# Kernel tuning notes

Hardware: AMD Instinct MI355X
Metric: run time of the kernel (lower is better)

Reference implementation:

```python
import jax, jax.numpy as jnp
import numpy as np

B, T, OBS, ACT, LAT = 64, 256, 512, 32, 64
BS, NB = 8, 8  # block side length, number of blocks (sum of sides == LAT)
PHI_OUT = NB * BS * BS


def setup_inputs() -> dict:
    key = jax.random.key(0)
    ks = jax.random.split(key, 6)
    w = lambda k, shape: jax.random.normal(k, shape, jnp.float32) * 0.05
    return {
        "observations": jax.random.normal(ks[0], (B, T, OBS), jnp.float32),
        "actions": jax.random.normal(ks[1], (B, T - 1, ACT), jnp.float32),
        "W_enc": w(ks[2], (OBS, LAT)),
        "b_enc": jnp.zeros((LAT,), jnp.float32),
        "W_dec": w(ks[3], (LAT, OBS)),
        "b_dec": jnp.zeros((OBS,), jnp.float32),
        "W_phi": w(ks[4], (ACT, PHI_OUT)),
        "b_phi": jnp.zeros((PHI_OUT,), jnp.float32),
    }


def _forward(observations, actions, W_enc, b_enc, W_dec, b_dec, W_phi, b_phi):
    Bb, Tt = observations.shape[:2]
    Ta = actions.shape[1]  # Tt - 1

    # h(o_t): encoder applied to flattened (B*T) observations
    latent_obs = (observations.reshape(Bb * Tt, OBS) @ W_enc + b_enc).reshape(Bb, Tt, LAT)

    # rho(g_t) = matrix_exp(block_diag(phi(g_t))). Since the matrix is exactly
    # block-diagonal (sum of block sides == LAT), expm factorizes per block.
    after_phi = actions.reshape(Bb * Ta, ACT) @ W_phi + b_phi  # (N, NB*BS*BS)
    # each block is reshaped (BS,BS) then transposed, as in the torch code
    blocks = after_phi.reshape(Bb * Ta * NB, BS, BS).transpose(0, 2, 1)
    exp_blocks = jax.vmap(jax.scipy.linalg.expm)(blocks)  # (N*NB, BS, BS)
    exp_blocks = exp_blocks.reshape(Bb * Ta, NB, BS, BS)
    rho = jnp.zeros((Bb * Ta, LAT, LAT), after_phi.dtype)
    for k in range(NB):  # small fixed structural loop over blocks
        rho = rho.at[:, k * BS:(k + 1) * BS, k * BS:(k + 1) * BS].set(exp_blocks[:, k])
    rho = rho.reshape(Bb, Ta, LAT, LAT)

    # sequential recurrence: h_{t} = h_{t-1} @ rho_{t-1} (row-vector times matrix)
    h0 = latent_obs[:, 0]  # (B, LAT)

    def step(h, rho_t):
        h_new = jnp.einsum('bl,blm->bm', h, rho_t)
        return h_new, h_new

    _, hs = jax.lax.scan(step, h0, jnp.swapaxes(rho, 0, 1))  # (Ta, B, LAT)
    predicted_latents = jnp.concatenate([h0[:, None], jnp.swapaxes(hs, 0, 1)], axis=1)  # (B, T, LAT)

    predicted_obs = (predicted_latents.reshape(Bb * Tt, LAT) @ W_dec + b_dec).reshape(Bb, Tt, OBS)
    return latent_obs, rho, predicted_latents, predicted_obs


def reference(observations, actions, W_enc, b_enc, W_dec, b_dec, W_phi, b_phi):
    return _forward(observations, actions, W_enc, b_enc, W_dec, b_dec, W_phi, b_phi)
```

## Files before the change

### kernel.cpp

```cpp
#include <hip/hip_runtime.h>

#define B_    64
#define T_    256
#define TA_   255
#define OBS_  512
#define ACT_  32
#define LAT_  64
#define NB_   8
#define BS_   8
#define PHI_  512
#define BT_   16384
#define BTA_  16320
#define CH_   16
#define NCH_  16

#define RHO_OFF   1048576ULL
#define PL_OFF    67895296ULL
#define POBS_OFF  68943872ULL

__global__ __launch_bounds__(256) void enc_kernel(
    const float* __restrict__ obs, const float* __restrict__ W,
    const float* __restrict__ bias, float* __restrict__ latent)
{
    __shared__ float At[64][68];
    __shared__ float Wt[64][64];
    const int tid = threadIdx.x;
    const int c0 = (tid & 15) * 4;
    const int r0 = (tid >> 4) * 4;
    const int row0 = blockIdx.x * 64;

    float4 pa[4], pw[4];
#pragma unroll
    for (int j = 0; j < 4; ++j) {
        int ft = tid + j * 256;
        int k4 = ft & 15, r = ft >> 4;
        pa[j] = *(const float4*)(obs + (size_t)(row0 + r) * OBS_ + k4 * 4);
        int c4 = ft & 15, kk = ft >> 4;
        pw[j] = *(const float4*)(W + (size_t)kk * LAT_ + c4 * 4);
    }

    float acc[4][4];
    float4 bv = *(const float4*)(bias + c0);
#pragma unroll
    for (int i = 0; i < 4; ++i) {
        acc[i][0] = bv.x; acc[i][1] = bv.y; acc[i][2] = bv.z; acc[i][3] = bv.w;
    }

    for (int kc = 0; kc < OBS_; kc += 64) {
#pragma unroll
        for (int j = 0; j < 4; ++j) {
            int ft = tid + j * 256;
            int k4 = ft & 15, r = ft >> 4;
            At[k4 * 4 + 0][r] = pa[j].x;
            At[k4 * 4 + 1][r] = pa[j].y;
            At[k4 * 4 + 2][r] = pa[j].z;
            At[k4 * 4 + 3][r] = pa[j].w;
            int c4 = ft & 15, kk = ft >> 4;
            *(float4*)(&Wt[kk][c4 * 4]) = pw[j];
        }
        __syncthreads();
        if (kc + 64 < OBS_) {
#pragma unroll
            for (int j = 0; j < 4; ++j) {
                int ft = tid + j * 256;
                int k4 = ft & 15, r = ft >> 4;
                pa[j] = *(const float4*)(obs + (size_t)(row0 + r) * OBS_ + kc + 64 + k4 * 4);
                int c4 = ft & 15, kk = ft >> 4;
                pw[j] = *(const float4*)(W + (size_t)(kc + 64 + kk) * LAT_ + c4 * 4);
            }
        }
#pragma unroll 4
        for (int kk = 0; kk < 64; ++kk) {
            float4 a = *(const float4*)(&At[kk][r0]);
            float4 w = *(const float4*)(&Wt[kk][c0]);
            acc[0][0] = fmaf(a.x, w.x, acc[0][0]); acc[0][1] = fmaf(a.x, w.y, acc[0][1]);
            acc[0][2] = fmaf(a.x, w.z, acc[0][2]); acc[0][3] = fmaf(a.x, w.w, acc[0][3]);
            acc[1][0] = fmaf(a.y, w.x, acc[1][0]); acc[1][1] = fmaf(a.y, w.y, acc[1][1]);
            acc[1][2] = fmaf(a.y, w.z, acc[1][2]); acc[1][3] = fmaf(a.y, w.w, acc[1][3]);
            acc[2][0] = fmaf(a.z, w.x, acc[2][0]); acc[2][1] = fmaf(a.z, w.y, acc[2][1]);
            acc[2][2] = fmaf(a.z, w.z, acc[2][2]); acc[2][3] = fmaf(a.z, w.w, acc[2][3]);
            acc[3][0] = fmaf(a.w, w.x, acc[3][0]); acc[3][1] = fmaf(a.w, w.y, acc[3][1]);
            acc[3][2] = fmaf(a.w, w.z, acc[3][2]); acc[3][3] = fmaf(a.w, w.w, acc[3][3]);
        }
        __syncthreads();
    }
#pragma unroll
    for (int i = 0; i < 4; ++i)
        *(float4*)(latent + (size_t)(row0 + r0 + i) * LAT_ + c0) =
            make_float4(acc[i][0], acc[i][1], acc[i][2], acc[i][3]);
}

__device__ __forceinline__ void mm8(float* __restrict__ D,
                                    const float* __restrict__ X,
                                    const float* __restrict__ Y)
{
#pragma unroll
    for (int r = 0; r < 8; ++r)
#pragma unroll
        for (int c = 0; c < 8; ++c) {
            float s = 0.f;
#pragma unroll
            for (int q = 0; q < 8; ++q) s = fmaf(X[r * 8 + q], Y[q * 8 + c], s);
            D[r * 8 + c] = s;
        }
}

__global__ __launch_bounds__(256, 1) void phi_expm_kernel(
    const float* __restrict__ act, const float* __restrict__ Wp,
    const float* __restrict__ bp, float* __restrict__ out_blocks,
    float* __restrict__ rho, int use_ws)
{
    const int bt = blockIdx.x * 256 + threadIdx.x;
    const int k  = blockIdx.y;
    if (bt >= BTA_) return;

    float A[64];
    {
        const float* bpp = bp + k * 64;
#pragma unroll
        for (int p = 0; p < 64; ++p) A[p] = bpp[p];
    }
    const float4* arow4 = (const float4*)(act + (size_t)bt * ACT_);
    const float* wk = Wp + k * 64;
#pragma unroll
    for (int a4 = 0; a4 < ACT_ / 4; ++a4) {
        float4 av = arow4[a4];
        const float* wr = wk + (size_t)(a4 * 4) * PHI_;
#pragma unroll
        for (int p = 0; p < 64; ++p) A[p] = fmaf(av.x, wr[p], A[p]);
        wr += PHI_;
#pragma unroll
        for (int p = 0; p < 64; ++p) A[p] = fmaf(av.y, wr[p], A[p]);
        wr += PHI_;
#pragma unroll
        for (int p = 0; p < 64; ++p) A[p] = fmaf(av.z, wr[p], A[p]);
        wr += PHI_;
#pragma unroll
        for (int p = 0; p < 64; ++p) A[p] = fmaf(av.w, wr[p], A[p]);
    }

#pragma unroll
    for (int r = 0; r < 8; ++r) {
        A[r * 9] *= 0.125f;
#pragma unroll
        for (int c = r + 1; c < 8; ++c) {
            float t = A[r * 8 + c];
            A[r * 8 + c] = 0.125f * A[c * 8 + r];
            A[c * 8 + r] = 0.125f * t;
        }
    }

    float P[64];
#pragma unroll
    for (int i = 0; i < 64; ++i) P[i] = (1.f / 5040.f) * A[i];
#pragma unroll
    for (int d = 0; d < 8; ++d) P[d * 9] += 1.f / 720.f;

    constexpr float COEF[6] = {1.f/120.f, 1.f/24.f, 1.f/6.f, 0.5f, 1.f, 1.f};
#pragma unroll
    for (int it = 0; it < 6; ++it) {
        const float coef = COEF[it];
#pragma unroll
        for (int r = 0; r < 8; ++r) {
            float t[8];
#pragma unroll
            for (int c = 0; c < 8; ++c) {
                float s = 0.f;
#pragma unroll
                for (int q = 0; q < 8; ++q) s = fmaf(P[r * 8 + q], A[q * 8 + c], s);
                t[c] = s;
            }
#pragma unroll
            for (int c = 0; c < 8; ++c) P[r * 8 + c] = t[c];
            P[r * 9] += coef;
        }
    }

    float T[64];
    mm8(T, P, P);
    mm8(P, T, T);
    mm8(T, P, P);

    if (use_ws) {
        float* dst = out_blocks + ((size_t)bt * NB_ + k) * 64;
#pragma unroll
        for (int i = 0; i < 16; ++i)
            ((float4*)dst)[i] = make_float4(T[4*i], T[4*i+1], T[4*i+2], T[4*i+3]);
    } else {
        float* base = rho + ((size_t)bt * LAT_ + k * BS_) * LAT_ + k * BS_;
#pragma unroll
        for (int r = 0; r < 8; ++r) {
            *(float4*)(base + (size_t)r * LAT_)     = make_float4(T[r*8+0], T[r*8+1], T[r*8+2], T[r*8+3]);
            *(float4*)(base + (size_t)r * LAT_ + 4) = make_float4(T[r*8+4], T[r*8+5], T[r*8+6], T[r*8+7]);
        }
    }
}

__global__ __launch_bounds__(256) void rho_write_kernel(
    const float* __restrict__ blocks, float* __restrict__ rho)
{
    size_t idx = (size_t)blockIdx.x * 256 + threadIdx.x;
    int c4 = (int)(idx & 15);
    size_t rowg = idx >> 4;
    int row = (int)(rowg & 63);
    size_t bt = rowg >> 6;
    int k = row >> 3, r = row & 7;
    float4 v = make_float4(0.f, 0.f, 0.f, 0.f);
    if ((c4 >> 1) == k)
        v = ((const float4*)(blocks + ((bt * 8 + (size_t)k) * 64 + (size_t)r * 8)))[c4 & 1];
    ((float4*)rho)[idx] = v;
}

__global__ __launch_bounds__(256) void zero_kernel(float4* __restrict__ p)
{
    p[(size_t)blockIdx.x * 256 + threadIdx.x] = make_float4(0.f, 0.f, 0.f, 0.f);
}

__global__ __launch_bounds__(256) void scan_local_kernel(
    const float* __restrict__ eb, float* __restrict__ pfx)
{
    const int tid = blockIdx.x * 256 + threadIdx.x;
    const int k = tid & 7;
    const int j = (tid >> 3) & 15;
    const int b = tid >> 7;
    const int t0 = j * CH_;
    const int cnt = (TA_ - t0 < CH_) ? (TA_ - t0) : CH_;
    const float* src = eb  + ((size_t)(b * TA_ + t0) * 8 + k) * 64;
    float*       dst = pfx + ((size_t)(b * TA_ + t0) * 8 + k) * 64;

    float R[64];
#pragma unroll
    for (int q = 0; q < 16; ++q) ((float4*)R)[q] = ((const float4*)src)[q];
#pragma unroll
    for (int q = 0; q < 16; ++q) ((float4*)dst)[q] = ((const float4*)R)[q];

    for (int i = 1; i < cnt; ++i) {
        const float* mp = src + (size_t)i * 512;
        float M[64];
#pragma unroll
        for (int q = 0; q < 16; ++q) ((float4*)M)[q] = ((const float4*)mp)[q];
#pragma unroll
        for (int r = 0; r < 8; ++r) {
            float tmp[8];
#pragma unroll
            for (int c = 0; c < 8; ++c) {
                float s = 0.f;
#pragma unroll
                for (int q = 0; q < 8; ++q) s = fmaf(R[r * 8 + q], M[q * 8 + c], s);
                tmp[c] = s;
            }
#pragma unroll
            for (int c = 0; c < 8; ++c) R[r * 8 + c] = tmp[c];
        }
        float* dp = dst + (size_t)i * 512;
#pragma unroll
        for (int q = 0; q < 16; ++q) ((float4*)dp)[q] = ((const float4*)R)[q];
    }
}

__global__ __launch_bounds__(64) void scan_chunk_kernel(
    const float* __restrict__ latent, const float* __restrict__ pfx,
    float* __restrict__ gws, float* __restrict__ pl)
{
    const int tid = blockIdx.x * 64 + threadIdx.x;
    const int k = tid & 7, b = tid >> 3;
    float g[8];
    const float* l0 = latent + (size_t)b * T_ * LAT_ + k * 8;
#pragma unroll
    for (int m = 0; m < 8; ++m) g[m] = l0[m];

    float* pl0 = pl + (size_t)b * T_ * LAT_ + k * 8;
    *(float4*)(pl0)     = make_float4(g[0], g[1], g[2], g[3]);
    *(float4*)(pl0 + 4) = make_float4(g[4], g[5], g[6], g[7]);

    float* gp = gws + ((size_t)(b * NCH_) * 8 + k) * 8;
    *(float4*)(gp)     = make_float4(g[0], g[1], g[2], g[3]);
    *(float4*)(gp + 4) = make_float4(g[4], g[5], g[6], g[7]);

    for (int j = 1; j < NCH_; ++j) {
        const float* cp = pfx + ((size_t)(b * TA_ + j * CH_ - 1) * 8 + k) * 64;
        float C[64];
#pragma unroll
        for (int q = 0; q < 16; ++q) ((float4*)C)[q] = ((const float4*)cp)[q];
        float ng[8];
#pragma unroll
        for (int m = 0; m < 8; ++m) {
            float s = 0.f;
#pragma unroll
            for (int l = 0; l < 8; ++l) s = fmaf(g[l], C[l * 8 + m], s);
            ng[m] = s;
        }
#pragma unroll
        for (int m = 0; m < 8; ++m) g[m] = ng[m];
        float* gq = gws + ((size_t)(b * NCH_ + j) * 8 + k) * 8;
        *(float4*)(gq)     = make_float4(g[0], g[1], g[2], g[3]);
        *(float4*)(gq + 4) = make_float4(g[4], g[5], g[6], g[7]);
    }
}

__global__ __launch_bounds__(256) void scan_emit_kernel(
    const float* __restrict__ pfx, const float* __restrict__ gws,
    float* __restrict__ pl)
{
    const int tid = blockIdx.x * 256 + threadIdx.x;
    const int k = tid & 7;
    const int bt = tid >> 3;
    const int b = bt / TA_;
    const int t = bt - b * TA_;
    const int j = t >> 4;

    float g[8];
    const float* gp = gws + ((size_t)(b * NCH_ + j) * 8 + k) * 8;
    *(float4*)(g)     = *(const float4*)(gp);
    *(float4*)(g + 4) = *(const float4*)(gp + 4);

    const float* lp = pfx + ((size_t)bt * 8 + k) * 64;
    float L[64];
#pragma unroll
    for (int q = 0; q < 16; ++q) ((float4*)L)[q] = ((const float4*)lp)[q];

    float h[8];
#pragma unroll
    for (int m = 0; m < 8; ++m) {
        float s = 0.f;
#pragma unroll
        for (int l = 0; l < 8; ++l) s = fmaf(g[l], L[l * 8 + m], s);
        h[m] = s;
    }
    float* op = pl + ((size_t)b * T_ + t + 1) * LAT_ + k * 8;
    *(float4*)(op)     = make_float4(h[0], h[1], h[2], h[3]);
    *(float4*)(op + 4) = make_float4(h[4], h[5], h[6], h[7]);
}

__device__ __forceinline__ void load_block8(float* __restrict__ dst,
                                            const float* __restrict__ p, int rs)
{
#pragma unroll
    for (int r = 0; r < 8; ++r) {
        float4 x = *(const float4*)(p + (size_t)r * rs);
        float4 y = *(const float4*)(p + (size_t)r * rs + 4);
        dst[r*8+0] = x.x; dst[r*8+1] = x.y; dst[r*8+2] = x.z; dst[r*8+3] = x.w;
        dst[r*8+4] = y.x; dst[r*8+5] = y.y; dst[r*8+6] = y.z; dst[r*8+7] = y.w;
    }
}

__global__ __launch_bounds__(64) void recur_kernel(
    const float* __restrict__ latent, const float* __restrict__ eb,
    int chainA, int chainB, int ts, int rs, float* __restrict__ pl)
{
    const int tid = blockIdx.x * 64 + threadIdx.x;
    const int b = tid >> 3, k = tid & 7;
    const float* e = eb + (size_t)b * (size_t)chainA + (size_t)k * (size_t)chainB;

    float h[8];
    const float* l0 = latent + (size_t)b * T_ * LAT_ + k * 8;
#pragma unroll
    for (int j = 0; j < 8; ++j) h[j] = l0[j];
    float* plp = pl + (size_t)b * T_ * LAT_ + k * 8;
    *(float4*)(plp)     = make_float4(h[0], h[1], h[2], h[3]);
    *(float4*)(plp + 4) = make_float4(h[4], h[5], h[6], h[7]);

    float eA[64], eB[64];
    load_block8(eA, e, rs);

#define STEP_(EBUF)                                                          \
    {                                                                        \
        float nh[8];                                                         \
        _Pragma("unroll")                                                    \
        for (int c = 0; c < 8; ++c) {                                        \
            float s = 0.f;                                                   \
            _Pragma("unroll")                                                \
            for (int r = 0; r < 8; ++r) s = fmaf(h[r], EBUF[r * 8 + c], s);  \
            nh[c] = s;                                                       \
        }                                                                    \
        plp += LAT_;                                                         \
        *(float4*)(plp)     = make_float4(nh[0], nh[1], nh[2], nh[3]);       \
        *(float4*)(plp + 4) = make_float4(nh[4], nh[5], nh[6], nh[7]);       \
        _Pragma("unroll")                                                    \
        for (int j = 0; j < 8; ++j) h[j] = nh[j];                            \
    }

    for (int t = 0; t < TA_; t += 2) {
        int tn = (t + 1 < TA_) ? t + 1 : TA_ - 1;
        load_block8(eB, e + (size_t)tn * ts, rs);
        STEP_(eA);
        if (t + 1 >= TA_) break;
        int tn2 = (t + 2 < TA_) ? t + 2 : TA_ - 1;
        load_block8(eA, e + (size_t)tn2 * ts, rs);
        STEP_(eB);
    }
#undef STEP_
}

__global__ __launch_bounds__(256) void dec_kernel(
    const float* __restrict__ pl, const float* __restrict__ W,
    const float* __restrict__ bias, float* __restrict__ out)
{
    __shared__ float At[64][68];
    __shared__ float Wt[64][64];
    const int tid = threadIdx.x;
    const int c0 = (tid & 15) * 4;
    const int r0 = (tid >> 4) * 4;
    const int row0 = blockIdx.x * 64;
    const int n0 = blockIdx.y * 64;

#pragma unroll
    for (int j = 0; j < 4; ++j) {
        int ft = tid + j * 256;
        int k4 = ft & 15, r = ft >> 4;
        float4 v = *(const float4*)(pl + (size_t)(row0 + r) * LAT_ + k4 * 4);
        At[k4 * 4 + 0][r] = v.x;
        At[k4 * 4 + 1][r] = v.y;
        At[k4 * 4 + 2][r] = v.z;
        At[k4 * 4 + 3][r] = v.w;
        int c4 = ft & 15, kk = ft >> 4;
        *(float4*)(&Wt[kk][c4 * 4]) =
            *(const float4*)(W + (size_t)kk * OBS_ + n0 + c4 * 4);
    }
    __syncthreads();

    float acc[4][4];
    float4 bv = *(const float4*)(bias + n0 + c0);
#pragma unroll
    for (int i = 0; i < 4; ++i) {
        acc[i][0] = bv.x; acc[i][1] = bv.y; acc[i][2] = bv.z; acc[i][3] = bv.w;
    }
#pragma unroll 4
    for (int kk = 0; kk < 64; ++kk) {
        float4 a = *(const float4*)(&At[kk][r0]);
        float4 w = *(const float4*)(&Wt[kk][c0]);
        acc[0][0] = fmaf(a.x, w.x, acc[0][0]); acc[0][1] = fmaf(a.x, w.y, acc[0][1]);
        acc[0][2] = fmaf(a.x, w.z, acc[0][2]); acc[0][3] = fmaf(a.x, w.w, acc[0][3]);
        acc[1][0] = fmaf(a.y, w.x, acc[1][0]); acc[1][1] = fmaf(a.y, w.y, acc[1][1]);
        acc[1][2] = fmaf(a.y, w.z, acc[1][2]); acc[1][3] = fmaf(a.y, w.w, acc[1][3]);
        acc[2][0] = fmaf(a.z, w.x, acc[2][0]); acc[2][1] = fmaf(a.z, w.y, acc[2][1]);
        acc[2][2] = fmaf(a.z, w.z, acc[2][2]); acc[2][3] = fmaf(a.z, w.w, acc[2][3]);
        acc[3][0] = fmaf(a.w, w.x, acc[3][0]); acc[3][1] = fmaf(a.w, w.y, acc[3][1]);
        acc[3][2] = fmaf(a.w, w.z, acc[3][2]); acc[3][3] = fmaf(a.w, w.w, acc[3][3]);
    }
#pragma unroll
    for (int i = 0; i < 4; ++i)
        *(float4*)(out + (size_t)(row0 + r0 + i) * OBS_ + n0 + c0) =
            make_float4(acc[i][0], acc[i][1], acc[i][2], acc[i][3]);
}

extern "C" void kernel_launch(void* const* d_in, const int* in_sizes, int n_in,
                              void* d_out, int out_size, void* d_ws, size_t ws_size,
                              hipStream_t stream)
{
    const float* obs  = (const float*)d_in[0];
    const float* act  = (const float*)d_in[1];
    const float* Wenc = (const float*)d_in[2];
    const float* benc = (const float*)d_in[3];
    const float* Wdec = (const float*)d_in[4];
    const float* bdec = (const float*)d_in[5];
    const float* Wphi = (const float*)d_in[6];
    const float* bphi = (const float*)d_in[7];

    float* out    = (float*)d_out;
    float* latent = out;
    float* rho    = out + RHO_OFF;
    float* pl     = out + PL_OFF;
    float* pobs   = out + POBS_OFF;

    const size_t eb_elems = (size_t)BTA_ * NB_ * 64;
    const size_t need_ws   = eb_elems * sizeof(float);
    const size_t need_scan = (2 * eb_elems + 512 * NCH_ * 8) * sizeof(float);
    const bool use_ws   = (ws_size >= need_ws);
    const bool use_scan = (ws_size >= need_scan);
    float* eb  = (float*)d_ws;
    float* pfx = eb + eb_elems;
    float* gws = pfx + eb_elems;

    hipLaunchKernelGGL(enc_kernel, dim3(BT_ / 64), dim3(256), 0, stream,
                       obs, Wenc, benc, latent);

    if (!use_ws)
        hipLaunchKernelGGL(zero_kernel, dim3(66846720 / 1024), dim3(256), 0, stream,
                           (float4*)rho);
    hipLaunchKernelGGL(phi_expm_kernel, dim3((BTA_ + 255) / 256, NB_), dim3(256), 0, stream,
                       act, Wphi, bphi, eb, rho, (int)use_ws);

    if (use_scan) {
        hipLaunchKernelGGL(scan_local_kernel, dim3(8192 / 256), dim3(256), 0, stream,
                           eb, pfx);
        hipLaunchKernelGGL(scan_chunk_kernel, dim3(8), dim3(64), 0, stream,
                           latent, pfx, gws, pl);
        hipLaunchKernelGGL(scan_emit_kernel, dim3(BTA_ * NB_ / 256), dim3(256), 0, stream,
                           pfx, gws, pl);
    } else if (use_ws) {
        hipLaunchKernelGGL(recur_kernel, dim3(8), dim3(64), 0, stream,
                           latent, eb, TA_ * 512, 64, 512, 8, pl);
    } else {
        hipLaunchKernelGGL(recur_kernel, dim3(8), dim3(64), 0, stream,
                           latent, rho, TA_ * 4096, BS_ * LAT_ + BS_, 4096, LAT_, pl);
    }

    if (use_ws)
        hipLaunchKernelGGL(rho_write_kernel, dim3(66846720 / 1024), dim3(256), 0, stream,
                           eb, rho);

    hipLaunchKernelGGL(dec_kernel, dim3(BT_ / 64, OBS_ / 64), dim3(256), 0, stream,
                       pl, Wdec, bdec, pobs);
}
```

Baseline: 523.9 us.

## Halve scan chunk size, fully unroll local scan, prefetch chunk carries

Shrinks the chunked scan from 16 chunks of 16 steps to 32 chunks of 8 steps, so the local-prefix kernel runs twice as many threads, each with a shorter serial dependency chain, in smaller 128-thread blocks. The fixed-length inner loop is fully unrolled via a macro, with a special case for the short last chunk. The sequential carry kernel now prefetches the next chunk matrix while multiplying the current one, hiding load latency. In exchange the serial carry pass has twice as many steps, and the launch-bounds changes may alter register allocation.

```diff
diff --git a/kernel.cpp b/kernel.cpp
--- a/kernel.cpp
+++ b/kernel.cpp
@@ -11,8 +11,8 @@
 #define PHI_  512
 #define BT_   16384
 #define BTA_  16320
-#define CH_   16
-#define NCH_  16
+#define CH_   8
+#define NCH_  32
 
 #define RHO_OFF   1048576ULL
 #define PL_OFF    67895296ULL
@@ -216,13 +216,38 @@
     p[(size_t)blockIdx.x * 256 + threadIdx.x] = make_float4(0.f, 0.f, 0.f, 0.f);
 }
 
-__global__ __launch_bounds__(256) void scan_local_kernel(
+#define SL_BODY_(I)                                                           \
+    {                                                                         \
+        const float* mp = src + (size_t)(I) * 512;                            \
+        float M[64];                                                          \
+        _Pragma("unroll")                                                     \
+        for (int q = 0; q < 16; ++q) ((float4*)M)[q] = ((const float4*)mp)[q];\
+        _Pragma("unroll")                                                     \
+        for (int r = 0; r < 8; ++r) {                                         \
+            float tmp[8];                                                     \
+            _Pragma("unroll")                                                 \
+            for (int c = 0; c < 8; ++c) {                                     \
+                float s = 0.f;                                                \
+                _Pragma("unroll")                                             \
+                for (int q = 0; q < 8; ++q)                                   \
+                    s = fmaf(R[r * 8 + q], M[q * 8 + c], s);                  \
+                tmp[c] = s;                                                   \
+            }                                                                 \
+            _Pragma("unroll")                                                 \
+            for (int c = 0; c < 8; ++c) R[r * 8 + c] = tmp[c];                \
+        }                                                                     \
+        float* dp = dst + (size_t)(I) * 512;                                  \
+        _Pragma("unroll")                                                     \
+        for (int q = 0; q < 16; ++q) ((float4*)dp)[q] = ((const float4*)R)[q];\
+    }
+
+__global__ __launch_bounds__(128, 1) void scan_local_kernel(
     const float* __restrict__ eb, float* __restrict__ pfx)
 {
-    const int tid = blockIdx.x * 256 + threadIdx.x;
+    const int tid = blockIdx.x * 128 + threadIdx.x;
     const int k = tid & 7;
-    const int j = (tid >> 3) & 15;
-    const int b = tid >> 7;
+    const int j = (tid >> 3) & 31;
+    const int b = tid >> 8;
     const int t0 = j * CH_;
     const int cnt = (TA_ - t0 < CH_) ? (TA_ - t0) : CH_;
     const float* src = eb  + ((size_t)(b * TA_ + t0) * 8 + k) * 64;
@@ -234,31 +259,17 @@
 #pragma unroll
     for (int q = 0; q < 16; ++q) ((float4*)dst)[q] = ((const float4*)R)[q];
 
-    for (int i = 1; i < cnt; ++i) {
-        const float* mp = src + (size_t)i * 512;
-        float M[64];
-#pragma unroll
-        for (int q = 0; q < 16; ++q) ((float4*)M)[q] = ((const float4*)mp)[q];
-#pragma unroll
-        for (int r = 0; r < 8; ++r) {
-            float tmp[8];
-#pragma unroll
-            for (int c = 0; c < 8; ++c) {
-                float s = 0.f;
-#pragma unroll
-                for (int q = 0; q < 8; ++q) s = fmaf(R[r * 8 + q], M[q * 8 + c], s);
-                tmp[c] = s;
-            }
-#pragma unroll
-            for (int c = 0; c < 8; ++c) R[r * 8 + c] = tmp[c];
-        }
-        float* dp = dst + (size_t)i * 512;
-#pragma unroll
-        for (int q = 0; q < 16; ++q) ((float4*)dp)[q] = ((const float4*)R)[q];
-    }
-}
-
-__global__ __launch_bounds__(64) void scan_chunk_kernel(
+    if (cnt == CH_) {
+#pragma unroll
+        for (int i = 1; i < CH_; ++i) SL_BODY_(i);
+    } else {
+#pragma unroll
+        for (int i = 1; i < CH_ - 1; ++i) SL_BODY_(i);
+    }
+}
+#undef SL_BODY_
+
+__global__ __launch_bounds__(64, 1) void scan_chunk_kernel(
     const float* __restrict__ latent, const float* __restrict__ pfx,
     float* __restrict__ gws, float* __restrict__ pl)
 {
@@ -277,11 +288,19 @@
     *(float4*)(gp)     = make_float4(g[0], g[1], g[2], g[3]);
     *(float4*)(gp + 4) = make_float4(g[4], g[5], g[6], g[7]);
 
+    float C[64];
+    {
+        const float* cp = pfx + ((size_t)(b * TA_ + CH_ - 1) * 8 + k) * 64;
+#pragma unroll
+        for (int q = 0; q < 16; ++q) ((float4*)C)[q] = ((const float4*)cp)[q];
+    }
     for (int j = 1; j < NCH_; ++j) {
-        const float* cp = pfx + ((size_t)(b * TA_ + j * CH_ - 1) * 8 + k) * 64;
-        float C[64];
-#pragma unroll
-        for (int q = 0; q < 16; ++q) ((float4*)C)[q] = ((const float4*)cp)[q];
+        float Cn[64];
+        if (j + 1 < NCH_) {
+            const float* cp = pfx + ((size_t)(b * TA_ + (j + 1) * CH_ - 1) * 8 + k) * 64;
+#pragma unroll
+            for (int q = 0; q < 16; ++q) ((float4*)Cn)[q] = ((const float4*)cp)[q];
+        }
         float ng[8];
 #pragma unroll
         for (int m = 0; m < 8; ++m) {
@@ -295,10 +314,12 @@
         float* gq = gws + ((size_t)(b * NCH_ + j) * 8 + k) * 8;
         *(float4*)(gq)     = make_float4(g[0], g[1], g[2], g[3]);
         *(float4*)(gq + 4) = make_float4(g[4], g[5], g[6], g[7]);
-    }
-}
-
-__global__ __launch_bounds__(256) void scan_emit_kernel(
+#pragma unroll
+        for (int q = 0; q < 64; ++q) C[q] = Cn[q];
+    }
+}
+
+__global__ __launch_bounds__(256, 1) void scan_emit_kernel(
     const float* __restrict__ pfx, const float* __restrict__ gws,
     float* __restrict__ pl)
 {
@@ -307,7 +328,7 @@
     const int bt = tid >> 3;
     const int b = bt / TA_;
     const int t = bt - b * TA_;
-    const int j = t >> 4;
+    const int j = t >> 3;
 
     float g[8];
     const float* gp = gws + ((size_t)(b * NCH_ + j) * 8 + k) * 8;
@@ -482,7 +503,7 @@
                        act, Wphi, bphi, eb, rho, (int)use_ws);
 
     if (use_scan) {
-        hipLaunchKernelGGL(scan_local_kernel, dim3(8192 / 256), dim3(256), 0, stream,
+        hipLaunchKernelGGL(scan_local_kernel, dim3(16384 / 128), dim3(128), 0, stream,
                            eb, pfx);
         hipLaunchKernelGGL(scan_chunk_kernel, dim3(8), dim3(64), 0, stream,
                            latent, pfx, gws, pl);
```

Result: faster. 499.2 us (-4.7%).
